# Kernel optimization log

Hardware: AMD Instinct MI355X
Metric: run time of the kernel (lower is better)

## Reference

```python
import jax, jax.numpy as jnp
import numpy as np

U, I, D, E = 50000, 100000, 64, 4000000
N = U + I
N_LAYERS = 3


def setup_inputs() -> dict:
    key = jax.random.key(0)
    k1, k2, k3, k4, k5 = jax.random.split(key, 5)
    user_emb = jax.random.normal(k1, (U, D), dtype=jnp.float32) * 0.1
    item_emb = jax.random.normal(k2, (I, D), dtype=jnp.float32) * 0.1
    edge_rows = jax.random.randint(k3, (E,), 0, N, dtype=jnp.int32)
    edge_cols = jax.random.randint(k4, (E,), 0, N, dtype=jnp.int32)
    # normalized-Laplacian-like positive values
    edge_vals = jax.random.uniform(k5, (E,), dtype=jnp.float32) * 0.01
    return {"user_emb": user_emb, "item_emb": item_emb,
            "edge_rows": edge_rows, "edge_cols": edge_cols,
            "edge_vals": edge_vals}


def _spmm(rows, cols, vals, x):
    # y[r] = sum_{e: rows[e]==r} vals[e] * x[cols[e]]   (COO SpMM)
    gathered = x[cols] * vals[:, None]          # [E, D]
    return jax.ops.segment_sum(gathered, rows, num_segments=N)


def reference(user_emb, item_emb, edge_rows, edge_cols, edge_vals):
    ego = jnp.concatenate([user_emb, item_emb], axis=0)  # [N, D]
    acc = ego
    for _ in range(N_LAYERS):
        ego = _spmm(edge_rows, edge_cols, edge_vals, ego)
        acc = acc + ego
    all_emb = acc / jnp.float32(N_LAYERS + 1)  # mean over stacked layer outputs
    return all_emb[:U], all_emb[U:]
```

## Files before the change

kernel.cpp:

```cpp
#include <hip/hip_runtime.h>
#include <hip/hip_fp16.h>

#define U_CNT 50000
#define I_CNT 100000
#define DIM 64
#define E_CNT 4000000
#define N_CNT (U_CNT + I_CNT)

#define BROWS 512
#define NBUK ((N_CNT + BROWS - 1) / BROWS)
#define CAP  16384
#define CHUNK_A 8192
#define NBLK_A ((E_CNT + CHUNK_A - 1) / CHUNK_A)
#define EPT (CHUNK_A / 512)

typedef unsigned long long u64;
typedef unsigned int u32;
typedef unsigned short u16;
typedef float f32x2 __attribute__((ext_vector_type(2)));
typedef _Float16 f16x2 __attribute__((ext_vector_type(2)));

__device__ __forceinline__ u16 f2h(float f) {
    return __half_as_ushort(__float2half(f));
}
__device__ __forceinline__ float h2f(u16 h) {
    return __half2float(__ushort_as_half(h));
}

__global__ __launch_bounds__(256) void init_kernel(
    const float* __restrict__ user_emb,
    const float* __restrict__ item_emb,
    u16* __restrict__ ego)
{
    long idx = (long)blockIdx.x * blockDim.x + threadIdx.x;
    const long total = (long)N_CNT * DIM / 4;
    if (idx >= total) return;
    long f = idx * 4;
    const long ubound = (long)U_CNT * DIM;
    float4 v;
    if (f < ubound) v = *(const float4*)(user_emb + f);
    else            v = *(const float4*)(item_emb + (f - ubound));
    ushort4 b;
    b.x = f2h(v.x); b.y = f2h(v.y); b.z = f2h(v.z); b.w = f2h(v.w);
    *(ushort4*)(ego + f) = b;
}

__global__ __launch_bounds__(512) void bucket_scatter(
    const int* __restrict__ rows, const int* __restrict__ cols,
    const float* __restrict__ vals, int* __restrict__ bucket_cursor,
    u64* __restrict__ pck1)
{
    __shared__ int hist[NBUK];
    __shared__ int base[NBUK];
    const int tid = threadIdx.x;
    if (tid < NBUK) hist[tid] = 0;
    __syncthreads();

    long e0 = (long)blockIdx.x * CHUNK_A;
    long e1 = e0 + CHUNK_A; if (e1 > E_CNT) e1 = E_CNT;

    u32 saved[EPT];
    int n = 0;
    for (long e = e0 + tid; e < e1; e += 512) {
        int r = rows[e];
        int b = r >> 9;
        int k = atomicAdd(&hist[b], 1);
        saved[n++] = ((u32)b << 22) | ((u32)(r & (BROWS - 1)) << 13) | (u32)k;
    }
    __syncthreads();

    if (tid < NBUK) {
        int h = hist[tid];
        base[tid] = h ? atomicAdd(&bucket_cursor[tid], h) : 0;
    }
    __syncthreads();

    n = 0;
    for (long e = e0 + tid; e < e1; e += 512) {
        u32 s = saved[n++];
        int b  = (int)(s >> 22);
        int rl = (int)((s >> 13) & (BROWS - 1));
        int k  = (int)(s & 8191);
        int pos = base[b] + k;
        if (pos < CAP) {
            u32 vcode = ((u32)f2h(vals[e]) >> 1) & 0x3FFFu;
            u64 packed = ((u64)vcode << 27) | ((u64)(u32)rl << 18) | (u32)cols[e];
            pck1[(long)b * CAP + pos] = packed;
        }
    }
}

__global__ __launch_bounds__(1024) void bucket_scan(
    const int* __restrict__ bucket_cursor, int* __restrict__ bucket_base)
{
    __shared__ int sm[1024];
    int tid = threadIdx.x;
    int c = (tid < NBUK) ? bucket_cursor[tid] : 0;
    int v = (c > CAP) ? CAP : c;
    sm[tid] = v;
    __syncthreads();
    for (int off = 1; off < 1024; off <<= 1) {
        int t = (tid >= off) ? sm[tid - off] : 0;
        __syncthreads();
        sm[tid] += t;
        __syncthreads();
    }
    if (tid < NBUK) bucket_base[tid] = sm[tid] - v;
}

__global__ __launch_bounds__(512) void bucket_sort(
    const u64* __restrict__ pck1,
    const int* __restrict__ bucket_cursor,
    const int* __restrict__ bucket_base,
    u32* __restrict__ pck,
    int* __restrict__ row_start)
{
    __shared__ int h[BROWS];
    __shared__ int sm[BROWS];
    __shared__ int cur[BROWS];
    const int b   = blockIdx.x;
    const int tid = threadIdx.x;
    int cnt = bucket_cursor[b]; if (cnt > CAP) cnt = CAP;
    const int S = bucket_base[b];
    const u64* src = pck1 + (long)b * CAP;

    h[tid] = 0;
    __syncthreads();
    for (int i = tid; i < cnt; i += 512)
        atomicAdd(&h[(int)((src[i] >> 18) & (BROWS - 1))], 1);
    __syncthreads();

    int v = h[tid];
    sm[tid] = v;
    __syncthreads();
    for (int off = 1; off < BROWS; off <<= 1) {
        int t = (tid >= off) ? sm[tid - off] : 0;
        __syncthreads();
        sm[tid] += t;
        __syncthreads();
    }
    int excl = sm[tid] - v;
    cur[tid] = excl;
    int idx = (b << 9) + tid;
    if (idx <= N_CNT) row_start[idx] = S + excl;
    __syncthreads();

    for (int i = tid; i < cnt; i += 512) {
        u64 pv = src[i];
        int rl = (int)((pv >> 18) & (BROWS - 1));
        int p = atomicAdd(&cur[rl], 1);
        pck[S + p] = (u32)(((pv >> 27) << 18) | (pv & 0x3FFFFu));
    }
}

__global__ __launch_bounds__(256) void spmm_csr(
    const int* __restrict__ row_start,
    const u32* __restrict__ pck,
    const u16* __restrict__ x,
    u16* __restrict__ y,
    float* __restrict__ outacc,
    int mode)
{
    const int lane = threadIdx.x & 63;
    const int g    = lane >> 3;
    const int h    = lane & 7;
    int r = (int)(((long)blockIdx.x * blockDim.x + threadIdx.x) >> 6);
    if (r >= N_CNT) return;
    int s = row_start[r];
    int e = row_start[r + 1];
    f32x2 A0 = {0.f, 0.f}, A1 = {0.f, 0.f}, A2 = {0.f, 0.f}, A3 = {0.f, 0.f};

#define EDGE_BODY(P)                                                        \
    {                                                                       \
        u32 c  = (P) & 0x3FFFFu;                                            \
        u32 hv = ((P) >> 17) & 0x7FFEu;                                     \
        u32 vv = hv | (hv << 16);                                           \
        f16x2 vh = __builtin_bit_cast(f16x2, vv);                           \
        const uint4 xb = *(const uint4*)(x + ((long)c << 6) + (h << 3));    \
        H0 += __builtin_bit_cast(f16x2, xb.x) * vh;                         \
        H1 += __builtin_bit_cast(f16x2, xb.y) * vh;                         \
        H2 += __builtin_bit_cast(f16x2, xb.z) * vh;                         \
        H3 += __builtin_bit_cast(f16x2, xb.w) * vh;                         \
    }

#define DO_ITERS(N)                                                         \
    {                                                                       \
        _Pragma("unroll")                                                   \
        for (int j = 0; j < (N); ++j) {                                     \
            u32 p = (u32)__shfl((int)pk, (j << 3) + g);                     \
            EDGE_BODY(p)                                                    \
        }                                                                   \
    }

    for (int base = s; base < e; base += 64) {
        int rem = e - base;
        u32 pk = 0u;
        if (base + lane < e) pk = __builtin_nontemporal_load(pck + base + lane);
        f16x2 H0 = {(_Float16)0, (_Float16)0}, H1 = H0, H2 = H0, H3 = H0;
        int it = (rem >= 64) ? 8 : ((rem + 7) >> 3);
        switch (it) {
            case 8: DO_ITERS(8) break;
            case 7: DO_ITERS(7) break;
            case 6: DO_ITERS(6) break;
            case 5: DO_ITERS(5) break;
            case 4: DO_ITERS(4) break;
            case 3: DO_ITERS(3) break;
            case 2: DO_ITERS(2) break;
            default: DO_ITERS(1) break;
        }
        #pragma unroll
        for (int off = 8; off < 64; off <<= 1) {
            H0 += __builtin_bit_cast(f16x2, (u32)__shfl_xor((int)__builtin_bit_cast(u32, H0), off));
            H1 += __builtin_bit_cast(f16x2, (u32)__shfl_xor((int)__builtin_bit_cast(u32, H1), off));
            H2 += __builtin_bit_cast(f16x2, (u32)__shfl_xor((int)__builtin_bit_cast(u32, H2), off));
            H3 += __builtin_bit_cast(f16x2, (u32)__shfl_xor((int)__builtin_bit_cast(u32, H3), off));
        }
        A0.x += (float)H0.x; A0.y += (float)H0.y;
        A1.x += (float)H1.x; A1.y += (float)H1.y;
        A2.x += (float)H2.x; A2.y += (float)H2.y;
        A3.x += (float)H3.x; A3.y += (float)H3.y;
    }
#undef DO_ITERS
#undef EDGE_BODY

    float a0 = A0.x, a1 = A0.y, a2 = A1.x, a3 = A1.y;
    float a4 = A2.x, a5 = A2.y, a6 = A3.x, a7 = A3.y;

    if (g == 0) {
        long o = ((long)r << 6) + (h << 3);
        if (mode < 2) {
            ushort4 y0, y1;
            y0.x = f2h(a0); y0.y = f2h(a1); y0.z = f2h(a2); y0.w = f2h(a3);
            y1.x = f2h(a4); y1.y = f2h(a5); y1.z = f2h(a6); y1.w = f2h(a7);
            *(ushort4*)(y + o)     = y0;
            *(ushort4*)(y + o + 4) = y1;
        }
        if (mode != 1) {
            const ushort4 xl = *(const ushort4*)(x + o);
            const ushort4 xh = *(const ushort4*)(x + o + 4);
            float o0 = h2f(xl.x), o1 = h2f(xl.y), o2 = h2f(xl.z), o3 = h2f(xl.w);
            float o4 = h2f(xh.x), o5 = h2f(xh.y), o6 = h2f(xh.z), o7 = h2f(xh.w);
            float4 t0, t1;
            if (mode == 0) {
                t0.x = o0 + a0; t0.y = o1 + a1; t0.z = o2 + a2; t0.w = o3 + a3;
                t1.x = o4 + a4; t1.y = o5 + a5; t1.z = o6 + a6; t1.w = o7 + a7;
            } else {
                t0 = *(const float4*)(outacc + o);
                t1 = *(const float4*)(outacc + o + 4);
                t0.x = (t0.x + o0 + a0) * 0.25f; t0.y = (t0.y + o1 + a1) * 0.25f;
                t0.z = (t0.z + o2 + a2) * 0.25f; t0.w = (t0.w + o3 + a3) * 0.25f;
                t1.x = (t1.x + o4 + a4) * 0.25f; t1.y = (t1.y + o5 + a5) * 0.25f;
                t1.z = (t1.z + o6 + a6) * 0.25f; t1.w = (t1.w + o7 + a7) * 0.25f;
            }
            *(float4*)(outacc + o)     = t0;
            *(float4*)(outacc + o + 4) = t1;
        }
    }
}

extern "C" void kernel_launch(void* const* d_in, const int* in_sizes, int n_in,
                              void* d_out, int out_size, void* d_ws, size_t ws_size,
                              hipStream_t stream) {
    const float* user_emb = (const float*)d_in[0];
    const float* item_emb = (const float*)d_in[1];
    const int*   rows     = (const int*)d_in[2];
    const int*   cols     = (const int*)d_in[3];
    const float* vals     = (const float*)d_in[4];
    float* outacc = (float*)d_out;

    char* ws = (char*)d_ws;
    u32*  pck  = (u32*)ws;                        ws += (size_t)E_CNT * 4;
    u64*  pck1 = (u64*)ws;
    u16*  ego  = (u16*)ws;
    u16*  nxt  = ego + (size_t)N_CNT * DIM;
    {
        size_t a = (size_t)NBUK * CAP * 8;
        size_t b = (size_t)N_CNT * DIM * 2 * 2;
        ws += (a > b) ? a : b;
    }
    int* row_start     = (int*)ws;                ws += (size_t)(N_CNT + 16) * 4;
    int* bucket_cursor = (int*)ws;                ws += 1024 * 4;
    int* bucket_base   = (int*)ws;                ws += 1024 * 4;

    hipMemsetAsync(bucket_cursor, 0, (size_t)NBUK * 4, stream);

    bucket_scatter<<<NBLK_A, 512, 0, stream>>>(rows, cols, vals, bucket_cursor, pck1);
    bucket_scan<<<1, 1024, 0, stream>>>(bucket_cursor, bucket_base);
    bucket_sort<<<NBUK, 512, 0, stream>>>(pck1, bucket_cursor, bucket_base, pck, row_start);

    const long total_f4 = (long)N_CNT * DIM / 4;
    const int  vgrid = (int)((total_f4 + 255) / 256);
    init_kernel<<<vgrid, 256, 0, stream>>>(user_emb, item_emb, ego);

    const int spmm_grid = (N_CNT * 64 + 255) / 256;
    spmm_csr<<<spmm_grid, 256, 0, stream>>>(row_start, pck, ego, nxt, outacc, 0);
    spmm_csr<<<spmm_grid, 256, 0, stream>>>(row_start, pck, nxt, ego, outacc, 1);
    spmm_csr<<<spmm_grid, 256, 0, stream>>>(row_start, pck, ego, nxt, outacc, 2);
}
```

Baseline: 319.9 us.

## Process two CSR rows per wavefront in the SpMM kernel

Each 64-lane wavefront now handles two consecutive rows, interleaving their 64-edge chunks in one loop and keeping two sets of accumulators. The grid is halved. The aim is more independent gathers in flight per wave and less per-row overhead for short rows (about 27 edges per row on average). The cost is more registers, lower occupancy, and idle lanes whenever the two rows differ in length.

```diff
diff --git a/kernel.cpp b/kernel.cpp
--- a/kernel.cpp
+++ b/kernel.cpp
@@ -164,70 +164,97 @@
     const int lane = threadIdx.x & 63;
     const int g    = lane >> 3;
     const int h    = lane & 7;
-    int r = (int)(((long)blockIdx.x * blockDim.x + threadIdx.x) >> 6);
-    if (r >= N_CNT) return;
-    int s = row_start[r];
-    int e = row_start[r + 1];
+    int w = (int)(((long)blockIdx.x * blockDim.x + threadIdx.x) >> 6);
+    if (w >= N_CNT / 2) return;
+    const int r0 = w << 1;
+    int s0  = row_start[r0];
+    int mid = row_start[r0 + 1];
+    int e1  = row_start[r0 + 2];
+
     f32x2 A0 = {0.f, 0.f}, A1 = {0.f, 0.f}, A2 = {0.f, 0.f}, A3 = {0.f, 0.f};
-
-#define EDGE_BODY(P)                                                        \
+    f32x2 B0 = {0.f, 0.f}, B1 = {0.f, 0.f}, B2 = {0.f, 0.f}, B3 = {0.f, 0.f};
+
+#define EDGE_BODY(P, Q0, Q1, Q2, Q3)                                        \
     {                                                                       \
         u32 c  = (P) & 0x3FFFFu;                                            \
         u32 hv = ((P) >> 17) & 0x7FFEu;                                     \
         u32 vv = hv | (hv << 16);                                           \
         f16x2 vh = __builtin_bit_cast(f16x2, vv);                           \
         const uint4 xb = *(const uint4*)(x + ((long)c << 6) + (h << 3));    \
-        H0 += __builtin_bit_cast(f16x2, xb.x) * vh;                         \
-        H1 += __builtin_bit_cast(f16x2, xb.y) * vh;                         \
-        H2 += __builtin_bit_cast(f16x2, xb.z) * vh;                         \
-        H3 += __builtin_bit_cast(f16x2, xb.w) * vh;                         \
-    }
-
-#define DO_ITERS(N)                                                         \
+        Q0 += __builtin_bit_cast(f16x2, xb.x) * vh;                         \
+        Q1 += __builtin_bit_cast(f16x2, xb.y) * vh;                         \
+        Q2 += __builtin_bit_cast(f16x2, xb.z) * vh;                         \
+        Q3 += __builtin_bit_cast(f16x2, xb.w) * vh;                         \
+    }
+
+#define DO_ITERS(N, PK, Q0, Q1, Q2, Q3)                                     \
     {                                                                       \
         _Pragma("unroll")                                                   \
         for (int j = 0; j < (N); ++j) {                                     \
-            u32 p = (u32)__shfl((int)pk, (j << 3) + g);                     \
-            EDGE_BODY(p)                                                    \
+            u32 p = (u32)__shfl((int)(PK), (j << 3) + g);                   \
+            EDGE_BODY(p, Q0, Q1, Q2, Q3)                                    \
         }                                                                   \
     }
 
-    for (int base = s; base < e; base += 64) {
-        int rem = e - base;
-        u32 pk = 0u;
-        if (base + lane < e) pk = __builtin_nontemporal_load(pck + base + lane);
-        f16x2 H0 = {(_Float16)0, (_Float16)0}, H1 = H0, H2 = H0, H3 = H0;
-        int it = (rem >= 64) ? 8 : ((rem + 7) >> 3);
-        switch (it) {
-            case 8: DO_ITERS(8) break;
-            case 7: DO_ITERS(7) break;
-            case 6: DO_ITERS(6) break;
-            case 5: DO_ITERS(5) break;
-            case 4: DO_ITERS(4) break;
-            case 3: DO_ITERS(3) break;
-            case 2: DO_ITERS(2) break;
-            default: DO_ITERS(1) break;
-        }
+#define ROW_CHUNK(REM, PK, Q0, Q1, Q2, Q3)                                  \
+    {                                                                       \
+        int it = ((REM) >= 64) ? 8 : (((REM) + 7) >> 3);                    \
+        switch (it) {                                                       \
+            case 8: DO_ITERS(8, PK, Q0, Q1, Q2, Q3) break;                  \
+            case 7: DO_ITERS(7, PK, Q0, Q1, Q2, Q3) break;                  \
+            case 6: DO_ITERS(6, PK, Q0, Q1, Q2, Q3) break;                  \
+            case 5: DO_ITERS(5, PK, Q0, Q1, Q2, Q3) break;                  \
+            case 4: DO_ITERS(4, PK, Q0, Q1, Q2, Q3) break;                  \
+            case 3: DO_ITERS(3, PK, Q0, Q1, Q2, Q3) break;                  \
+            case 2: DO_ITERS(2, PK, Q0, Q1, Q2, Q3) break;                  \
+            default: DO_ITERS(1, PK, Q0, Q1, Q2, Q3) break;                 \
+        }                                                                   \
+    }
+
+    int base0 = s0, base1 = mid;
+    while (base0 < mid || base1 < e1) {
+        int rem0 = mid - base0;
+        int rem1 = e1 - base1;
+        u32 pk0 = 0u, pk1 = 0u;
+        if (base0 + lane < mid) pk0 = __builtin_nontemporal_load(pck + base0 + lane);
+        if (base1 + lane < e1)  pk1 = __builtin_nontemporal_load(pck + base1 + lane);
+        f16x2 Hz = {(_Float16)0, (_Float16)0};
+        f16x2 H0 = Hz, H1 = Hz, H2 = Hz, H3 = Hz;
+        f16x2 K0 = Hz, K1 = Hz, K2 = Hz, K3 = Hz;
+        if (rem0 > 0) ROW_CHUNK(rem0, pk0, H0, H1, H2, H3)
+        if (rem1 > 0) ROW_CHUNK(rem1, pk1, K0, K1, K2, K3)
         #pragma unroll
         for (int off = 8; off < 64; off <<= 1) {
             H0 += __builtin_bit_cast(f16x2, (u32)__shfl_xor((int)__builtin_bit_cast(u32, H0), off));
             H1 += __builtin_bit_cast(f16x2, (u32)__shfl_xor((int)__builtin_bit_cast(u32, H1), off));
             H2 += __builtin_bit_cast(f16x2, (u32)__shfl_xor((int)__builtin_bit_cast(u32, H2), off));
             H3 += __builtin_bit_cast(f16x2, (u32)__shfl_xor((int)__builtin_bit_cast(u32, H3), off));
+            K0 += __builtin_bit_cast(f16x2, (u32)__shfl_xor((int)__builtin_bit_cast(u32, K0), off));
+            K1 += __builtin_bit_cast(f16x2, (u32)__shfl_xor((int)__builtin_bit_cast(u32, K1), off));
+            K2 += __builtin_bit_cast(f16x2, (u32)__shfl_xor((int)__builtin_bit_cast(u32, K2), off));
+            K3 += __builtin_bit_cast(f16x2, (u32)__shfl_xor((int)__builtin_bit_cast(u32, K3), off));
         }
         A0.x += (float)H0.x; A0.y += (float)H0.y;
         A1.x += (float)H1.x; A1.y += (float)H1.y;
         A2.x += (float)H2.x; A2.y += (float)H2.y;
         A3.x += (float)H3.x; A3.y += (float)H3.y;
-    }
+        B0.x += (float)K0.x; B0.y += (float)K0.y;
+        B1.x += (float)K1.x; B1.y += (float)K1.y;
+        B2.x += (float)K2.x; B2.y += (float)K2.y;
+        B3.x += (float)K3.x; B3.y += (float)K3.y;
+        base0 += 64; base1 += 64;
+    }
+#undef ROW_CHUNK
 #undef DO_ITERS
 #undef EDGE_BODY
 
-    float a0 = A0.x, a1 = A0.y, a2 = A1.x, a3 = A1.y;
-    float a4 = A2.x, a5 = A2.y, a6 = A3.x, a7 = A3.y;
-
-    if (g == 0) {
-        long o = ((long)r << 6) + (h << 3);
+    float a0 = g ? B0.x : A0.x, a1 = g ? B0.y : A0.y;
+    float a2 = g ? B1.x : A1.x, a3 = g ? B1.y : A1.y;
+    float a4 = g ? B2.x : A2.x, a5 = g ? B2.y : A2.y;
+    float a6 = g ? B3.x : A3.x, a7 = g ? B3.y : A3.y;
+
+    if (g < 2) {
+        long o = ((long)(r0 + g) << 6) + (h << 3);
         if (mode < 2) {
             ushort4 y0, y1;
             y0.x = f2h(a0); y0.y = f2h(a1); y0.z = f2h(a2); y0.w = f2h(a3);
@@ -292,7 +319,7 @@
     const int  vgrid = (int)((total_f4 + 255) / 256);
     init_kernel<<<vgrid, 256, 0, stream>>>(user_emb, item_emb, ego);
 
-    const int spmm_grid = (N_CNT * 64 + 255) / 256;
+    const int spmm_grid = ((N_CNT / 2) * 64 + 255) / 256;
     spmm_csr<<<spmm_grid, 256, 0, stream>>>(row_start, pck, ego, nxt, outacc, 0);
     spmm_csr<<<spmm_grid, 256, 0, stream>>>(row_start, pck, nxt, ego, outacc, 1);
     spmm_csr<<<spmm_grid, 256, 0, stream>>>(row_start, pck, ego, nxt, outacc, 2);
```

Result: no change. 318.5 us (-0.4%).
